# Optimization experiments

Measured on AMD Instinct MI355X. Metric: run time of the kernel, lower is better.

## Reference

```python
import jax, jax.numpy as jnp
import numpy as np

B, S, D, H = 2, 2048, 4096, 32
Dh = D // H          # 128, rotary_dim == head_dim
BASE = 10000.0       # rope_theta
SCALE = Dh ** -0.5


def setup_inputs() -> dict:
    key = jax.random.key(0)
    k0, k1, k2 = jax.random.split(key, 3)
    w_scale = 0.02
    return {
        "hidden_states": jax.random.normal(k0, (B, S, D), jnp.float32),
        "positions": jnp.broadcast_to(jnp.arange(S, dtype=jnp.int32), (B, S)),
        "Wqkv": jax.random.normal(k1, (D, 3 * D), jnp.float32) * w_scale,
        "bqkv": jnp.zeros((3 * D,), jnp.float32),
        "Wproj": jax.random.normal(k2, (D, D), jnp.float32) * w_scale,
    }


def _apply_rope(x, positions):
    # x: [B, S, H, Dh]; neox-style (rotate-half) RoPE, as in vLLM PagedAttentionWithRoPE
    half = Dh // 2
    inv_freq = 1.0 / (BASE ** (jnp.arange(half, dtype=jnp.float32) / half))
    ang = positions[..., None].astype(jnp.float32) * inv_freq      # [B, S, half]
    cos = jnp.cos(ang)[:, :, None, :]                              # [B, S, 1, half]
    sin = jnp.sin(ang)[:, :, None, :]
    x1, x2 = x[..., :half], x[..., half:]
    return jnp.concatenate([x1 * cos - x2 * sin, x2 * cos + x1 * sin], axis=-1)


def reference(hidden_states, positions, Wqkv, bqkv, Wproj):
    # c_attn: fused QKV projection
    qkv = hidden_states @ Wqkv + bqkv                              # [B, S, 3D]
    q, k, v = jnp.split(qkv, 3, axis=-1)
    q = q.reshape(B, S, H, Dh)
    k = k.reshape(B, S, H, Dh)
    v = v.reshape(B, S, H, Dh)
    # fused RoPE on q and k at the given positions
    q = _apply_rope(q, positions)
    k = _apply_rope(k, positions)
    # causal scaled-dot-product attention (prefill semantics of paged attention)
    scores = jnp.einsum("bqhd,bkhd->bhqk", q, k) * SCALE           # [B, H, S, S]
    causal = jnp.tril(jnp.ones((S, S), dtype=bool))
    scores = jnp.where(causal, scores, jnp.finfo(scores.dtype).min)
    attn = jax.nn.softmax(scores, axis=-1)
    ctx = jnp.einsum("bhqk,bkhd->bqhd", attn, v).reshape(B, S, D)
    # c_proj (no bias)
    return ctx @ Wproj
```

## Files before the change

kernel.cpp:

```cpp
#include <hip/hip_runtime.h>

typedef __attribute__((ext_vector_type(8))) short short8;
typedef __attribute__((ext_vector_type(4))) short short4v;
typedef __attribute__((ext_vector_type(4))) float f32x4;

#define LDS8(base, off) (*(const short8*)((const char*)(base) + (off)))
#define GLOAD_LDS16(gp, lp) __builtin_amdgcn_global_load_lds( \
    (const __attribute__((address_space(1))) unsigned int*)(gp), \
    (__attribute__((address_space(3))) unsigned int*)(lp), 16, 0, 0)
#define SBAR() __builtin_amdgcn_s_barrier()
#define SB0() __builtin_amdgcn_sched_barrier(0)

__device__ __forceinline__ short f2bf(float f) {
    unsigned u = __builtin_bit_cast(unsigned, f);
    unsigned r = (u + 0x7FFFu + ((u >> 16) & 1u)) >> 16;
    return (short)r;
}
__device__ __forceinline__ float bf2f(short s) {
    unsigned u = ((unsigned)(unsigned short)s) << 16;
    return __builtin_bit_cast(float, u);
}

__global__ __launch_bounds__(256) void cvt_f32_bf16(const float* __restrict__ in,
                                                    short* __restrict__ out, int n8) {
    int i = blockIdx.x * 256 + threadIdx.x;
    if (i < n8) {
        const f32x4* p = (const f32x4*)(in + (size_t)i * 8);
        f32x4 a = p[0], bq = p[1];
        short8 o;
        o[0] = f2bf(a[0]); o[1] = f2bf(a[1]); o[2] = f2bf(a[2]); o[3] = f2bf(a[3]);
        o[4] = f2bf(bq[0]); o[5] = f2bf(bq[1]); o[6] = f2bf(bq[2]); o[7] = f2bf(bq[3]);
        *(short8*)(out + (size_t)i * 8) = o;
    }
}

__global__ __launch_bounds__(256) void transpose_cvt(const float* __restrict__ W,
                                                     short* __restrict__ Out, int R, int C) {
    __shared__ float tile[64][33];
    int c0 = blockIdx.x * 64, r0 = blockIdx.y * 32;
    int tid = threadIdx.x;
    int cc4 = (tid & 15) * 4;
#pragma unroll
    for (int it = 0; it < 2; ++it) {
        int rr = (tid >> 4) + it * 16;
        f32x4 v = *(const f32x4*)&W[(size_t)(r0 + rr) * C + c0 + cc4];
#pragma unroll
        for (int i = 0; i < 4; ++i) tile[cc4 + i][rr] = v[i];
    }
    __syncthreads();
    int cc = tid >> 2, r8 = (tid & 3) * 8;
    short8 o;
#pragma unroll
    for (int i = 0; i < 8; ++i) o[i] = f2bf(tile[cc][r8 + i]);
    *(short8*)&Out[(size_t)(c0 + cc) * R + r0 + r8] = o;
}

__global__ __launch_bounds__(256) void rope_table(float* __restrict__ ctab, float* __restrict__ stab) {
    int idx = blockIdx.x * 256 + threadIdx.x;
    int t = idx >> 6, j = idx & 63;
    float inv = expf(-(float)j * (9.210340371976184f / 64.0f));
    float ang = (float)t * inv;
    ctab[idx] = cosf(ang);
    stab[idx] = sinf(ang);
}

__global__ __launch_bounds__(256) void rope_scatter(const short* __restrict__ qkv,
                                                    const int* __restrict__ pos,
                                                    const float* __restrict__ ctab,
                                                    const float* __restrict__ stab,
                                                    short* __restrict__ Q, short* __restrict__ K) {
    int id = blockIdx.x * 256 + threadIdx.x;
    int j = id & 63;
    int h = (id >> 6) & 31;
    int s = (id >> 11) & 2047;
    int b = id >> 22;
    size_t qrow = (size_t)(b * 2048 + s) * 12288 + h * 128;
    float q1 = bf2f(qkv[qrow + j]),        q2 = bf2f(qkv[qrow + 64 + j]);
    float k1 = bf2f(qkv[qrow + 4096 + j]), k2 = bf2f(qkv[qrow + 4160 + j]);
    int p = pos[b * 2048 + s];
    float c = ctab[p * 64 + j], si = stab[p * 64 + j];
    size_t orow = ((size_t)(b * 32 + h) * 2048 + s) * 128;
    Q[orow + j]      = f2bf(q1 * c - q2 * si);
    Q[orow + 64 + j] = f2bf(q2 * c + q1 * si);
    K[orow + j]      = f2bf(k1 * c - k2 * si);
    K[orow + 64 + j] = f2bf(k2 * c + k1 * si);
}

__global__ __launch_bounds__(256) void v_transpose(const short* __restrict__ qkv,
                                                   short* __restrict__ Vt) {
    int bh = blockIdx.z; int b = bh >> 5, h = bh & 31;
    int s0 = blockIdx.x * 64, d0 = blockIdx.y * 64;
    __shared__ short tile[64][65];
    int tid = threadIdx.x;
    int sl = tid >> 3;
    int d8 = (tid & 7) * 8;
#pragma unroll
    for (int it = 0; it < 2; ++it) {
        int s = sl + it * 32;
        short8 v = *(const short8*)&qkv[(size_t)(b * 2048 + s0 + s) * 12288 + 8192 + h * 128 + d0 + d8];
#pragma unroll
        for (int i = 0; i < 8; ++i) tile[s][d8 + i] = v[i];
    }
    __syncthreads();
    int dl = tid >> 3;
    int s8 = (tid & 7) * 8;
#pragma unroll
    for (int it = 0; it < 2; ++it) {
        int d = dl + it * 32;
        short8 o;
#pragma unroll
        for (int i = 0; i < 8; ++i) o[i] = tile[s8 + i][d];
        *(short8*)&Vt[((size_t)bh * 128 + d0 + d) * 2048 + s0 + s8] = o;
    }
}

__global__ __launch_bounds__(512, 2) void gemm256(const short* __restrict__ A,
                                                  const short* __restrict__ Bt,
                                                  const float* __restrict__ bias,
                                                  short* __restrict__ Cbf,
                                                  float* __restrict__ Cf,
                                                  int M, int N, int K, int nN) {
    __shared__ __align__(16) char smem[131072];
    const int tid = threadIdx.x;
    const int l = tid & 63, w = tid >> 6;
    const int m = l & 15, g = l >> 4, m7 = m & 7;
    const int wm = w >> 2, wn = w & 3;

    int cpx = gridDim.x >> 3;
    int wg = (blockIdx.x & 7) * cpx + (blockIdx.x >> 3);
    int gsz = nN << 3;
    int grp = wg / gsz, rem = wg - grp * gsz;
    int bm = (grp << 3) + (rem & 7);
    int bn = rem >> 3;
    int m0 = bm << 8, n0 = bn << 8;

    const int srow = l >> 3;
    const int sgcol = ((l & 7) ^ srow) << 3;

    const int NT = K >> 6;

    const int AbaseR = wm << 14;
    const int BbaseR = 32768 + ((wn >> 1) << 14);
    const int brow0 = (wn & 1) << 6;

    f32x4 acc[8][4];
    const f32x4 fz = {0.f, 0.f, 0.f, 0.f};
#pragma unroll
    for (int i = 0; i < 8; ++i)
#pragma unroll
        for (int j = 0; j < 4; ++j) acc[i][j] = fz;

    auto stage_half = [&](const short* G, int grow0, int kcol, int ldsoff) {
        GLOAD_LDS16(G + (size_t)(grow0 +      w * 8 + srow) * K + kcol + sgcol,
                    smem + ldsoff + w * 1024);
        GLOAD_LDS16(G + (size_t)(grow0 + 64 + w * 8 + srow) * K + kcol + sgcol,
                    smem + ldsoff + 8192 + w * 1024);
    };

    short8 afX[2][2], afY[2][2], bf[4][2];

#define RD_AF(DST, I0)                                                           \
    _Pragma("unroll")                                                            \
    for (int i2 = 0; i2 < 2; ++i2) {                                             \
        _Pragma("unroll")                                                        \
        for (int kk = 0; kk < 2; ++kk)                                           \
            DST[i2][kk] = LDS8(Ab, (((I0) + i2) * 16 + m) * 128 + (((kk * 4 + g) ^ m7) << 4)); \
    }

#define MFMA_IP(IP, AF)                                                          \
    do {                                                                         \
        __builtin_amdgcn_s_setprio(1);                                           \
        _Pragma("unroll")                                                        \
        for (int kk = 0; kk < 2; ++kk) {                                         \
            _Pragma("unroll")                                                    \
            for (int i2 = 0; i2 < 2; ++i2) {                                     \
                _Pragma("unroll")                                                \
                for (int j2 = 0; j2 < 4; ++j2) {                                 \
                    acc[(IP) * 2 + i2][j2] = __builtin_amdgcn_mfma_f32_16x16x32_bf16( \
                        AF[i2][kk], bf[j2][kk], acc[(IP) * 2 + i2][j2], 0, 0, 0); \
                }                                                                \
            }                                                                    \
        }                                                                        \
        __builtin_amdgcn_s_setprio(0);                                           \
    } while (0)

#pragma unroll
    for (int t = 0; t < 2; ++t) {
        int sb = t << 16;
        stage_half(A,  m0,       t * 64, sb);
        stage_half(A,  m0 + 128, t * 64, sb + 16384);
        stage_half(Bt, n0,       t * 64, sb + 32768);
        stage_half(Bt, n0 + 128, t * 64, sb + 49152);
    }
    asm volatile("s_waitcnt vmcnt(8)");
    SB0();
    SBAR();

    for (int kt = 0; kt < NT; ++kt) {
        const int slotb = (kt & 1) << 16;
        const char* Ab = smem + slotb + AbaseR;
        const char* Bb = smem + slotb + BbaseR;
        const bool pf = (kt + 2) < NT;
        const int kc = (kt + 2) << 6;

#pragma unroll
        for (int j = 0; j < 4; ++j) {
#pragma unroll
            for (int kk = 0; kk < 2; ++kk)
                bf[j][kk] = LDS8(Bb, (brow0 + j * 16 + m) * 128 + (((kk * 4 + g) ^ m7) << 4));
        }
        RD_AF(afX, 0);
        RD_AF(afY, 2);
        SB0();
        asm volatile("s_waitcnt lgkmcnt(4)");
        SB0();
        MFMA_IP(0, afX);
        RD_AF(afX, 4);
        SB0();
        asm volatile("s_waitcnt lgkmcnt(4)");
        SB0();
        MFMA_IP(1, afY);
        RD_AF(afY, 6);
        SB0();
        asm volatile("s_waitcnt lgkmcnt(4)");
        SB0();
        MFMA_IP(2, afX);
        asm volatile("s_waitcnt lgkmcnt(0)");
        SB0();
        MFMA_IP(3, afY);

        SBAR();
        if (pf) {
            stage_half(A,  m0,       kc, slotb);
            stage_half(A,  m0 + 128, kc, slotb + 16384);
            stage_half(Bt, n0,       kc, slotb + 32768);
            stage_half(Bt, n0 + 128, kc, slotb + 49152);
        }
        if (kt + 1 < NT) {
            if (pf) asm volatile("s_waitcnt vmcnt(8)");
            else    asm volatile("s_waitcnt vmcnt(0)");
            SB0();
            SBAR();
        }
    }
#undef RD_AF
#undef MFMA_IP

#pragma unroll
    for (int i = 0; i < 8; ++i) {
#pragma unroll
        for (int j = 0; j < 4; ++j) {
#pragma unroll
            for (int r = 0; r < 4; ++r) {
                int row = m0 + wm * 128 + i * 16 + g * 4 + r;
                int col = n0 + wn * 64 + j * 16 + m;
                float v = acc[i][j][r];
                if (bias) v += bias[col];
                if (Cbf) Cbf[(size_t)row * N + col] = f2bf(v);
                else     Cf[(size_t)row * N + col] = v;
            }
        }
    }
}

__global__ __launch_bounds__(512, 4) void flash_fwd(const short* __restrict__ Q,
                                                    const short* __restrict__ Kt,
                                                    const short* __restrict__ Vt,
                                                    short* __restrict__ ctx) {
    const int S = 2048;
    const float SCALE = 0.08838834764831845f;
    __shared__ __align__(16) char smem[81920];

    int tid = threadIdx.x, l = tid & 63, w = tid >> 6;
    int m = l & 15, g = l >> 4, m7 = m & 7;
    int qg = blockIdx.x, h = blockIdx.y, b = blockIdx.z;
    int bh = b * 32 + h;
    int q0 = qg * 128 + w * 16;

    const short* Qg = Q + ((size_t)bh * S + q0) * 128;
    const short* Kg = Kt + (size_t)bh * S * 128;
    const short* Vg = Vt + (size_t)bh * 128 * S;

    short8 qf[4];
#pragma unroll
    for (int kb = 0; kb < 4; ++kb)
        qf[kb] = *(const short8*)(Qg + m * 128 + kb * 32 + g * 8);

    const f32x4 fz = {0.f, 0.f, 0.f, 0.f};
    f32x4 O[8];
#pragma unroll
    for (int nb = 0; nb < 8; ++nb) O[nb] = fz;
    float Mr[4], Lr[4];
#pragma unroll
    for (int r = 0; r < 4; ++r) { Mr[r] = -__builtin_inff(); Lr[r] = 0.f; }

    const short* Kp[2]; const short* Vp[2]; int KlO[2], VlO[2];
#pragma unroll
    for (int q = 0; q < 2; ++q) {
        int c = w * 2 + q;
        int rowK = c * 4 + (l >> 4);
        Kp[q] = Kg + (size_t)rowK * 128 + (((l & 15) ^ (rowK & 7)) * 8);
        KlO[q] = c * 1024;
        int rowV = c * 8 + (l >> 3);
        Vp[q] = Vg + (size_t)rowV * S + (((l & 7) ^ (rowV & 7)) * 8);
        VlO[q] = c * 1024;
    }

    auto stage = [&](int t, int slot) {
#pragma unroll
        for (int q = 0; q < 2; ++q) {
            GLOAD_LDS16(Kp[q] + (size_t)t * 8192, smem + slot * 16384 + KlO[q]);
            GLOAD_LDS16(Vp[q] + t * 64, smem + 32768 + slot * 16384 + VlO[q]);
        }
    };

    int nkt = 2 * qg + 2;
    stage(0, 0);
    asm volatile("s_waitcnt vmcnt(0)");
    SB0();
    SBAR();

    for (int kt = 0; kt < nkt; ++kt) {
        if (kt + 1 < nkt) stage(kt + 1, (kt + 1) & 1);
        const char* Kl = smem + (kt & 1) * 16384;
        const char* Vl = smem + 32768 + (kt & 1) * 16384;
        char* Pl = smem + 65536 + w * 2048;
        int k0 = kt * 64;
        if (k0 <= q0 + 15) {
            f32x4 sc[4];
#pragma unroll
            for (int j = 0; j < 4; ++j) sc[j] = fz;
#pragma unroll
            for (int kb = 0; kb < 4; ++kb) {
#pragma unroll
                for (int j = 0; j < 4; ++j) {
                    short8 kf = LDS8(Kl, (j * 16 + m) * 256 + (((kb * 4 + g) ^ m7) << 4));
                    sc[j] = __builtin_amdgcn_mfma_f32_16x16x32_bf16(qf[kb], kf, sc[j], 0, 0, 0);
                }
            }
            bool diag = (k0 + 63 > q0);
#pragma unroll
            for (int r = 0; r < 4; ++r) {
                int qrow = q0 + g * 4 + r;
                float s0 = sc[0][r] * SCALE;
                float s1 = sc[1][r] * SCALE;
                float s2 = sc[2][r] * SCALE;
                float s3 = sc[3][r] * SCALE;
                if (diag) {
                    if (k0 + m > qrow)      s0 = -__builtin_inff();
                    if (k0 + 16 + m > qrow) s1 = -__builtin_inff();
                    if (k0 + 32 + m > qrow) s2 = -__builtin_inff();
                    if (k0 + 48 + m > qrow) s3 = -__builtin_inff();
                }
                float mx = fmaxf(fmaxf(s0, s1), fmaxf(s2, s3));
                mx = fmaxf(mx, __shfl_xor(mx, 1, 64));
                mx = fmaxf(mx, __shfl_xor(mx, 2, 64));
                mx = fmaxf(mx, __shfl_xor(mx, 4, 64));
                mx = fmaxf(mx, __shfl_xor(mx, 8, 64));
                float mnew = fmaxf(Mr[r], mx);
                float alpha = __expf(Mr[r] - mnew);
                float p0 = __expf(s0 - mnew);
                float p1 = __expf(s1 - mnew);
                float p2 = __expf(s2 - mnew);
                float p3 = __expf(s3 - mnew);
                float rs = (p0 + p1) + (p2 + p3);
                rs += __shfl_xor(rs, 1, 64);
                rs += __shfl_xor(rs, 2, 64);
                rs += __shfl_xor(rs, 4, 64);
                rs += __shfl_xor(rs, 8, 64);
                Lr[r] = Lr[r] * alpha + rs;
                Mr[r] = mnew;
#pragma unroll
                for (int nb = 0; nb < 8; ++nb) O[nb][r] *= alpha;
                int pr = g * 4 + r;
                char* pw = Pl + pr * 128;
                float pv[4] = {p0, p1, p2, p3};
#pragma unroll
                for (int j = 0; j < 4; ++j) {
                    int lb = j * 32 + m * 2;
                    int pb = (((lb >> 4) ^ (pr & 7)) << 4) | (lb & 15);
                    *(short*)(pw + pb) = f2bf(pv[j]);
                }
            }
            short8 pf[2];
#pragma unroll
            for (int kh = 0; kh < 2; ++kh)
                pf[kh] = LDS8(Pl, m * 128 + (((kh * 4 + g) ^ m7) << 4));
#pragma unroll
            for (int kh = 0; kh < 2; ++kh) {
#pragma unroll
                for (int nb = 0; nb < 8; ++nb) {
                    int d = nb * 16 + m;
                    short8 vf = LDS8(Vl, d * 128 + (((kh * 4 + g) ^ m7) << 4));
                    O[nb] = __builtin_amdgcn_mfma_f32_16x16x32_bf16(pf[kh], vf, O[nb], 0, 0, 0);
                }
            }
        }
        if (kt + 1 < nkt) {
            asm volatile("s_waitcnt vmcnt(0)");
            SB0();
            SBAR();
        }
    }
#pragma unroll
    for (int nb = 0; nb < 8; ++nb) {
#pragma unroll
        for (int r = 0; r < 4; ++r) {
            int row = q0 + g * 4 + r;
            float v = O[nb][r] / Lr[r];
            ctx[(size_t)(b * S + row) * 4096 + h * 128 + nb * 16 + m] = f2bf(v);
        }
    }
}

extern "C" void kernel_launch(void* const* d_in, const int* in_sizes, int n_in,
                              void* d_out, int out_size, void* d_ws, size_t ws_size,
                              hipStream_t stream) {
    const float* hidden    = (const float*)d_in[0];
    const int*   positions = (const int*)d_in[1];
    const float* Wqkv      = (const float*)d_in[2];
    const float* bqkv      = (const float*)d_in[3];
    const float* Wproj     = (const float*)d_in[4];
    float* out = (float*)d_out;
    char* ws = (char*)d_ws;

    short* Abf    = (short*)(ws + 0ull);
    short* WqkvT  = (short*)(ws + 33554432ull);
    short* WprojT = (short*)(ws + 134217728ull);
    short* qkv    = (short*)(ws + 167772160ull);
    short* Qr     = (short*)(ws + 268435456ull);
    short* Kr     = (short*)(ws + 301989888ull);
    short* Vt     = (short*)(ws + 335544320ull);
    short* ctx    = (short*)(ws + 369098752ull);
    float* ctab   = (float*)(ws + 402653184ull);
    float* stab   = (float*)(ws + 403177472ull);

    cvt_f32_bf16<<<8192, 256, 0, stream>>>(hidden, Abf, 2097152);
    transpose_cvt<<<dim3(192, 128), 256, 0, stream>>>(Wqkv, WqkvT, 4096, 12288);
    transpose_cvt<<<dim3(64, 128), 256, 0, stream>>>(Wproj, WprojT, 4096, 4096);
    rope_table<<<512, 256, 0, stream>>>(ctab, stab);
    gemm256<<<dim3(768), 512, 0, stream>>>(Abf, WqkvT, bqkv, qkv, nullptr, 4096, 12288, 4096, 48);
    rope_scatter<<<32768, 256, 0, stream>>>(qkv, positions, ctab, stab, Qr, Kr);
    v_transpose<<<dim3(32, 2, 64), 256, 0, stream>>>(qkv, Vt);
    flash_fwd<<<dim3(16, 32, 2), 512, 0, stream>>>(Qr, Kr, Vt, ctx);
    gemm256<<<dim3(256), 512, 0, stream>>>(ctx, WprojT, nullptr, nullptr, out, 4096, 4096, 4096, 16);
}
```

Baseline: 937.2 us.

## Prefetch next-tile GEMM fragments early and split attention K/V waits with lazy rescale

In the GEMM main loop, the B fragments and first A fragments for the next k-tile are now read from LDS right after the barrier, before the current tile's last MFMA group finishes. The global prefetch is issued after those reads, so LDS read latency overlaps with MFMA work. In the attention kernel, K and V staging are split so the score and softmax phase waits only on K, and V is waited for just before the PV MFMAs. The online softmax now rescales O and L only when the running max grows by more than a threshold, which skips most rescale multiplies. Changing the wait counts and reusing slots raises the risk of LDS hazards and of subtle precision effects from the lazy max.

```diff
diff --git a/kernel.cpp b/kernel.cpp
--- a/kernel.cpp
+++ b/kernel.cpp
@@ -136,7 +136,6 @@
 
     const int srow = l >> 3;
     const int sgcol = ((l & 7) ^ srow) << 3;
-
     const int NT = K >> 6;
 
     const int AbaseR = wm << 14;
@@ -159,14 +158,20 @@
 
     short8 afX[2][2], afY[2][2], bf[4][2];
 
-#define RD_AF(DST, I0)                                                           \
+#define RD_AF(DST, BASE, I0)                                                     \
     _Pragma("unroll")                                                            \
     for (int i2 = 0; i2 < 2; ++i2) {                                             \
         _Pragma("unroll")                                                        \
         for (int kk = 0; kk < 2; ++kk)                                           \
-            DST[i2][kk] = LDS8(Ab, (((I0) + i2) * 16 + m) * 128 + (((kk * 4 + g) ^ m7) << 4)); \
-    }
-
+            DST[i2][kk] = LDS8(BASE, (((I0) + i2) * 16 + m) * 128 + (((kk * 4 + g) ^ m7) << 4)); \
+    }
+#define RD_BF(BASE)                                                              \
+    _Pragma("unroll")                                                            \
+    for (int j2 = 0; j2 < 4; ++j2) {                                             \
+        _Pragma("unroll")                                                        \
+        for (int kk = 0; kk < 2; ++kk)                                           \
+            bf[j2][kk] = LDS8(BASE, (brow0 + j2 * 16 + m) * 128 + (((kk * 4 + g) ^ m7) << 4)); \
+    }
 #define MFMA_IP(IP, AF)                                                          \
     do {                                                                         \
         __builtin_amdgcn_s_setprio(1);                                           \
@@ -195,55 +200,50 @@
     asm volatile("s_waitcnt vmcnt(8)");
     SB0();
     SBAR();
+    {
+        const char* Ab0 = smem + AbaseR;
+        const char* Bb0 = smem + BbaseR;
+        RD_BF(Bb0);
+        RD_AF(afX, Ab0, 0);
+        SB0();
+    }
 
     for (int kt = 0; kt < NT; ++kt) {
-        const int slotb = (kt & 1) << 16;
-        const char* Ab = smem + slotb + AbaseR;
-        const char* Bb = smem + slotb + BbaseR;
+        const int slotb  = (kt & 1) << 16;
+        const int slotbN = ((kt + 1) & 1) << 16;
+        const char* Ab  = smem + slotb + AbaseR;
+        const char* AbN = smem + slotbN + AbaseR;
+        const char* BbN = smem + slotbN + BbaseR;
+        const bool nx = (kt + 1) < NT;
         const bool pf = (kt + 2) < NT;
         const int kc = (kt + 2) << 6;
 
-#pragma unroll
-        for (int j = 0; j < 4; ++j) {
-#pragma unroll
-            for (int kk = 0; kk < 2; ++kk)
-                bf[j][kk] = LDS8(Bb, (brow0 + j * 16 + m) * 128 + (((kk * 4 + g) ^ m7) << 4));
-        }
-        RD_AF(afX, 0);
-        RD_AF(afY, 2);
-        SB0();
-        asm volatile("s_waitcnt lgkmcnt(4)");
-        SB0();
+        RD_AF(afY, Ab, 2); SB0();
+        asm volatile("s_waitcnt lgkmcnt(4)"); SB0();
         MFMA_IP(0, afX);
-        RD_AF(afX, 4);
-        SB0();
-        asm volatile("s_waitcnt lgkmcnt(4)");
-        SB0();
+        RD_AF(afX, Ab, 4); SB0();
+        asm volatile("s_waitcnt lgkmcnt(4)"); SB0();
         MFMA_IP(1, afY);
-        RD_AF(afY, 6);
-        SB0();
-        asm volatile("s_waitcnt lgkmcnt(4)");
-        SB0();
+        RD_AF(afY, Ab, 6); SB0();
+        asm volatile("s_waitcnt lgkmcnt(4)"); SB0();
         MFMA_IP(2, afX);
-        asm volatile("s_waitcnt lgkmcnt(0)");
-        SB0();
+        asm volatile("s_waitcnt lgkmcnt(0)"); SB0();
+        asm volatile("s_waitcnt vmcnt(0)"); SB0();
+        SBAR();
         MFMA_IP(3, afY);
-
-        SBAR();
-        if (pf) {
-            stage_half(A,  m0,       kc, slotb);
-            stage_half(A,  m0 + 128, kc, slotb + 16384);
-            stage_half(Bt, n0,       kc, slotb + 32768);
-            stage_half(Bt, n0 + 128, kc, slotb + 49152);
-        }
-        if (kt + 1 < NT) {
-            if (pf) asm volatile("s_waitcnt vmcnt(8)");
-            else    asm volatile("s_waitcnt vmcnt(0)");
-            SB0();
-            SBAR();
+        if (nx) {
+            RD_BF(BbN); SB0();
+            RD_AF(afX, AbN, 0); SB0();
+            if (pf) {
+                stage_half(A,  m0,       kc, slotb);
+                stage_half(A,  m0 + 128, kc, slotb + 16384);
+                stage_half(Bt, n0,       kc, slotb + 32768);
+                stage_half(Bt, n0 + 128, kc, slotb + 49152);
+            }
         }
     }
 #undef RD_AF
+#undef RD_BF
 #undef MFMA_IP
 
 #pragma unroll
@@ -306,27 +306,32 @@
         VlO[q] = c * 1024;
     }
 
-    auto stage = [&](int t, int slot) {
-#pragma unroll
-        for (int q = 0; q < 2; ++q) {
+    auto stageK = [&](int t, int slot) {
+#pragma unroll
+        for (int q = 0; q < 2; ++q)
             GLOAD_LDS16(Kp[q] + (size_t)t * 8192, smem + slot * 16384 + KlO[q]);
+    };
+    auto stageV = [&](int t, int slot) {
+#pragma unroll
+        for (int q = 0; q < 2; ++q)
             GLOAD_LDS16(Vp[q] + t * 64, smem + 32768 + slot * 16384 + VlO[q]);
-        }
     };
 
     int nkt = 2 * qg + 2;
-    stage(0, 0);
-    asm volatile("s_waitcnt vmcnt(0)");
+    stageK(0, 0); stageV(0, 0);
+    asm volatile("s_waitcnt vmcnt(2)");
     SB0();
     SBAR();
 
     for (int kt = 0; kt < nkt; ++kt) {
-        if (kt + 1 < nkt) stage(kt + 1, (kt + 1) & 1);
-        const char* Kl = smem + (kt & 1) * 16384;
-        const char* Vl = smem + 32768 + (kt & 1) * 16384;
+        int slot = kt & 1;
+        if (kt + 1 < nkt) { stageK(kt + 1, slot ^ 1); stageV(kt + 1, slot ^ 1); }
+        const char* Kl = smem + slot * 16384;
+        const char* Vl = smem + 32768 + slot * 16384;
         char* Pl = smem + 65536 + w * 2048;
         int k0 = kt * 64;
-        if (k0 <= q0 + 15) {
+        bool comp = (k0 <= q0 + 15);
+        if (comp) {
             f32x4 sc[4];
 #pragma unroll
             for (int j = 0; j < 4; ++j) sc[j] = fz;
@@ -357,21 +362,23 @@
                 mx = fmaxf(mx, __shfl_xor(mx, 2, 64));
                 mx = fmaxf(mx, __shfl_xor(mx, 4, 64));
                 mx = fmaxf(mx, __shfl_xor(mx, 8, 64));
-                float mnew = fmaxf(Mr[r], mx);
-                float alpha = __expf(Mr[r] - mnew);
-                float p0 = __expf(s0 - mnew);
-                float p1 = __expf(s1 - mnew);
-                float p2 = __expf(s2 - mnew);
-                float p3 = __expf(s3 - mnew);
+                if (mx > Mr[r] + 8.0f) {
+                    float alpha = __expf(Mr[r] - mx);
+                    Lr[r] *= alpha;
+#pragma unroll
+                    for (int nb = 0; nb < 8; ++nb) O[nb][r] *= alpha;
+                    Mr[r] = mx;
+                }
+                float p0 = __expf(s0 - Mr[r]);
+                float p1 = __expf(s1 - Mr[r]);
+                float p2 = __expf(s2 - Mr[r]);
+                float p3 = __expf(s3 - Mr[r]);
                 float rs = (p0 + p1) + (p2 + p3);
                 rs += __shfl_xor(rs, 1, 64);
                 rs += __shfl_xor(rs, 2, 64);
                 rs += __shfl_xor(rs, 4, 64);
                 rs += __shfl_xor(rs, 8, 64);
-                Lr[r] = Lr[r] * alpha + rs;
-                Mr[r] = mnew;
-#pragma unroll
-                for (int nb = 0; nb < 8; ++nb) O[nb][r] *= alpha;
+                Lr[r] += rs;
                 int pr = g * 4 + r;
                 char* pw = Pl + pr * 128;
                 float pv[4] = {p0, p1, p2, p3};
@@ -382,6 +389,12 @@
                     *(short*)(pw + pb) = f2bf(pv[j]);
                 }
             }
+        }
+        if (kt + 1 < nkt) asm volatile("s_waitcnt vmcnt(4)");
+        else              asm volatile("s_waitcnt vmcnt(0)");
+        SB0();
+        SBAR();
+        if (comp) {
             short8 pf[2];
 #pragma unroll
             for (int kh = 0; kh < 2; ++kh)
@@ -397,7 +410,7 @@
             }
         }
         if (kt + 1 < nkt) {
-            asm volatile("s_waitcnt vmcnt(0)");
+            asm volatile("s_waitcnt vmcnt(2)");
             SB0();
             SBAR();
         }
```

After: 900.9 us. 3.9% less time.
